# Performance work log

Hardware: AMD Instinct MI355X
Metric: run time of the kernel (lower is better)

Reference implementation:

```python
import jax, jax.numpy as jnp
import numpy as np

ROLLBACK = 1  # rollback_range: warp at 2**rollback finer resolution, then downsample
B, C, H, W = 2, 32, 512, 512
CIN = 3 * (C // 2) + 2  # inner module input channels


def _bilinear_warp(img, res):
    """Bilinear gather. img: [B,Cc,Hh,Ww]; res: [B,Hh,Ww,2] pixel offsets (x,y).
    Samples img at (x+res_x, y+res_y) with zero padding outside."""
    Bb, Cc, Hh, Ww = img.shape
    gy, gx = jnp.meshgrid(jnp.arange(Hh, dtype=img.dtype),
                          jnp.arange(Ww, dtype=img.dtype), indexing='ij')
    sx = gx[None] + res[..., 0]  # [B,Hh,Ww]
    sy = gy[None] + res[..., 1]
    x0 = jnp.floor(sx); y0 = jnp.floor(sy)
    wx = sx - x0; wy = sy - y0

    def gather(yi, xi):
        inb = ((yi >= 0) & (yi < Hh) & (xi >= 0) & (xi < Ww)).astype(img.dtype)
        yc = jnp.clip(yi, 0, Hh - 1).astype(jnp.int32)
        xc = jnp.clip(xi, 0, Ww - 1).astype(jnp.int32)
        v = jax.vmap(lambda im, y, x: im[:, y, x])(img, yc, xc)  # [B,Cc,Hh,Ww]
        return v * inb[:, None]

    v00 = gather(y0, x0);     v01 = gather(y0, x0 + 1)
    v10 = gather(y0 + 1, x0); v11 = gather(y0 + 1, x0 + 1)
    wx = wx[:, None]; wy = wy[:, None]  # broadcast over channels
    return (v00 * (1 - wy) * (1 - wx) + v01 * (1 - wy) * wx
            + v10 * wy * (1 - wx) + v11 * wy * wx)


def _resize_img(img, f):  # [B,Cc,Hh,Ww] bilinear spatial resize
    Bb, Cc, Hh, Ww = img.shape
    return jax.image.resize(img, (Bb, Cc, int(Hh * f), int(Ww * f)), 'bilinear')


def _resize_res(res, f):  # [B,Hh,Ww,2]; pixel-unit values scale with resolution
    Bb, Hh, Ww, _ = res.shape
    return jax.image.resize(res, (Bb, int(Hh * f), int(Ww * f), 2), 'bilinear') * f


def res_warp_img(img, res, rollback):
    if rollback > 0:
        f = 2 ** rollback
        out = _bilinear_warp(_resize_img(img, f), _resize_res(res, f))
        return _resize_img(out, 1.0 / f)
    return _bilinear_warp(img, res)


def res_warp_res(res_a, res_b, rollback):
    # warp residual field a (treated as a 2-channel image, values in pixel units) by b
    if rollback > 0:
        f = 2 ** rollback
        a = _resize_res(res_a, f); b = _resize_res(res_b, f)
        out = jnp.transpose(_bilinear_warp(jnp.transpose(a, (0, 3, 1, 2)), b), (0, 2, 3, 1))
        return _resize_res(out, 1.0 / f)
    out = _bilinear_warp(jnp.transpose(res_a, (0, 3, 1, 2)), res_b)
    return jnp.transpose(out, (0, 2, 3, 1))


def combine_residuals(res_a, res_b, rollback):
    # flow composition: apply a then b
    return res_b + res_warp_res(res_a, res_b, rollback)


def _conv3x3(x, w, b):
    y = jax.lax.conv_general_dilated(x, w, (1, 1), 'SAME',
                                     dimension_numbers=('NCHW', 'OIHW', 'NCHW'))
    return y + b[None, :, None, None]


def setup_inputs() -> dict:
    key = jax.random.key(0)
    k1, k2, k3 = jax.random.split(key, 3)
    x = jax.random.normal(k1, (B, C, H, W), dtype=jnp.float32)
    res = jax.random.normal(k2, (B, 2, H, W), dtype=jnp.float32)  # ~1px flow
    W_inner = jax.random.normal(k3, (2, CIN, 3, 3), dtype=jnp.float32) * 0.02
    b_inner = jnp.zeros((2,), dtype=jnp.float32)
    return {"x": x, "res": res, "W_inner": W_inner, "b_inner": b_inner, "level": 0}


def reference(x, res, W_inner, b_inner, level):
    res_hw = jnp.transpose(res, (0, 2, 3, 1))  # [B,H,W,2]
    nf = x.shape[1]
    src, tgt = x[:, :nf // 2], x[:, nf // 2:]
    warped_tgt = res_warp_img(tgt, res_hw, ROLLBACK)
    bundle = jnp.concatenate([src, tgt, warped_tgt, res], axis=1)  # [B,3C/2+2,H,W]
    adj = _conv3x3(bundle, W_inner, b_inner)  # hindsight_adjustment [B,2,H,W]
    # mode == 'combine_res': state['down'][level]['input'] = combined residual
    new_res = combine_residuals(res_hw, jnp.transpose(adj, (0, 2, 3, 1)), ROLLBACK)
    hindsight_warped_tgt = res_warp_img(tgt, new_res, ROLLBACK)
    return jnp.concatenate([src, hindsight_warped_tgt], axis=1)  # [B,C,H,W]
```

## Files before the change

### kernel.cpp

```cpp
#include <hip/hip_runtime.h>
#include <hip/hip_bf16.h>
#include <cstdint>
#include <cstddef>

#define HW   512
#define HW2  1024
#define SZ   (512 * 512)
#define NPT  (34 * 34)
#define K_PTS 5
#define SRCW 36
#define SRCP 37
#define NSRC (SRCW * SRCW)
#define MARG 9

struct UpTap { int i0, i1; float w0, w1; };

__device__ __forceinline__ UpTap up_tap(int i) {
  UpTap t;
  int k = i >> 1;
  if ((i & 1) == 0) {
    t.i0 = k - 1; t.i1 = k; t.w0 = 0.25f; t.w1 = 0.75f;
    if (k == 0) { t.i0 = 0; t.w0 = 0.0f; t.w1 = 1.0f; }
  } else {
    t.i0 = k; t.i1 = k + 1; t.w0 = 0.75f; t.w1 = 0.25f;
    if (k == HW - 1) { t.i1 = HW - 1; t.w0 = 1.0f; t.w1 = 0.0f; }
  }
  return t;
}

__device__ __forceinline__ float up_at(const float* __restrict__ plane, int yi, int xi) {
  UpTap ty = up_tap(yi), tx = up_tap(xi);
  const float* r0 = plane + (size_t)ty.i0 * HW;
  const float* r1 = plane + (size_t)ty.i1 * HW;
  float v00 = r0[tx.i0], v01 = r0[tx.i1];
  float v10 = r1[tx.i0], v11 = r1[tx.i1];
  return ty.w0 * (tx.w0 * v00 + tx.w1 * v01) + ty.w1 * (tx.w0 * v10 + tx.w1 * v11);
}

__device__ __forceinline__ void axis_taps(float s, int& base, float& w0, float& w1, float& w2) {
  float f0 = floorf(s);
  int i0 = (int)f0;
  float fr = s - f0;
  int b = (i0 & 1) ? (i0 >> 1) : (i0 >> 1) - 1;
  b = b < 0 ? 0 : (b > (HW - 3) ? (HW - 3) : b);
  float w[3] = {0.0f, 0.0f, 0.0f};
  if ((unsigned)i0 < (unsigned)HW2) {
    UpTap t = up_tap(i0);
    w[t.i0 - b] += (1.0f - fr) * t.w0;
    w[t.i1 - b] += (1.0f - fr) * t.w1;
  }
  if ((unsigned)(i0 + 1) < (unsigned)HW2) {
    UpTap t = up_tap(i0 + 1);
    w[t.i0 - b] += fr * t.w0;
    w[t.i1 - b] += fr * t.w1;
  }
  base = b; w0 = w[0]; w1 = w[1]; w2 = w[2];
}

__global__ void copy_src_kernel(const float* __restrict__ x, float* __restrict__ out) {
  const size_t half = (size_t)16 * SZ;
  const size_t nvec = half / 4;
  size_t i = (size_t)blockIdx.x * blockDim.x + threadIdx.x;
  if (i < 2 * nvec) {
    size_t b = i / nvec, j = i % nvec;
    const float4* s = (const float4*)(x + b * 2 * half);
    float4* d = (float4*)(out + b * 2 * half);
    d[j] = s[j];
  }
}

struct PtTaps {
  int   locoff;
  float wy0, wy1, wy2, wx0, wx1, wx2;
};

__device__ __forceinline__ void compute_taps(const float* __restrict__ fx,
                                             const float* __restrict__ fy,
                                             int gx0, int gy0, int xo, int yo, int tid,
                                             PtTaps (&pt)[K_PTS]) {
  #pragma unroll
  for (int i = 0; i < K_PTS; ++i) {
    int p = tid + i * 256;
    pt[i].locoff = 0;
    pt[i].wy0 = pt[i].wy1 = pt[i].wy2 = 0.0f;
    pt[i].wx0 = pt[i].wx1 = pt[i].wx2 = 0.0f;
    if (p < NPT) {
      int ry = p / 34, rx = p % 34;
      int yy = gy0 + ry, xx = gx0 + rx;
      if ((unsigned)yy < (unsigned)HW2 && (unsigned)xx < (unsigned)HW2) {
        float sx = (float)xx + 2.0f * up_at(fx, yy, xx);
        float sy = (float)yy + 2.0f * up_at(fy, yy, xx);
        int bx, by;
        axis_taps(sx, bx, pt[i].wx0, pt[i].wx1, pt[i].wx2);
        axis_taps(sy, by, pt[i].wy0, pt[i].wy1, pt[i].wy2);
        int rx_ = bx - xo, ry_ = by - yo;
        if ((unsigned)rx_ <= (unsigned)(SRCW - 3) && (unsigned)ry_ <= (unsigned)(SRCW - 3))
          pt[i].locoff = ry_ * SRCP + rx_;
        else
          pt[i].locoff = ~(by * HW + bx);
      }
    }
  }
}

__device__ __forceinline__ void stage_pair(const float* __restrict__ p0,
                                           const float* __restrict__ p1,
                                           float* __restrict__ s0,
                                           float* __restrict__ s1,
                                           int xo, int yo, int tid) {
  #pragma unroll
  for (int i = 0; i < 6; ++i) {
    int p = tid + i * 256;
    if (p < NSRC) {
      int r = p / SRCW, c = p % SRCW;
      int gy = yo + r; gy = gy < 0 ? 0 : (gy > HW - 1 ? HW - 1 : gy);
      int gx = xo + c; gx = gx < 0 ? 0 : (gx > HW - 1 ? HW - 1 : gx);
      size_t o = (size_t)gy * HW + gx;
      int d = r * SRCP + c;
      s0[d] = p0[o];
      s1[d] = p1[o];
    }
  }
}

__device__ __forceinline__ float eval3_global(const float* __restrict__ pl, int off, const PtTaps& t) {
  const float* p0 = pl + off;
  float r0 = t.wx0 * p0[0]        + t.wx1 * p0[1]          + t.wx2 * p0[2];
  float r1 = t.wx0 * p0[HW]       + t.wx1 * p0[HW + 1]     + t.wx2 * p0[HW + 2];
  float r2 = t.wx0 * p0[2 * HW]   + t.wx1 * p0[2 * HW + 1] + t.wx2 * p0[2 * HW + 2];
  return t.wy0 * r0 + t.wy1 * r1 + t.wy2 * r2;
}

__device__ __forceinline__ void eval_round(const float* __restrict__ s0,
                                           const float* __restrict__ s1,
                                           float* __restrict__ t0,
                                           float* __restrict__ t1,
                                           const float* __restrict__ plane0,
                                           const float* __restrict__ plane1,
                                           const PtTaps (&pt)[K_PTS], int tid) {
  #pragma unroll
  for (int i = 0; i < K_PTS; ++i) {
    int p = tid + i * 256;
    if (p < NPT) {
      const PtTaps t = pt[i];
      float a0, a1;
      if (t.locoff >= 0) {
        const float* a = s0 + t.locoff;
        const float* b = s1 + t.locoff;
        float r00 = t.wx0 * a[0]        + t.wx1 * a[1]            + t.wx2 * a[2];
        float r10 = t.wx0 * a[SRCP]     + t.wx1 * a[SRCP + 1]     + t.wx2 * a[SRCP + 2];
        float r20 = t.wx0 * a[2 * SRCP] + t.wx1 * a[2 * SRCP + 1] + t.wx2 * a[2 * SRCP + 2];
        float r01 = t.wx0 * b[0]        + t.wx1 * b[1]            + t.wx2 * b[2];
        float r11 = t.wx0 * b[SRCP]     + t.wx1 * b[SRCP + 1]     + t.wx2 * b[SRCP + 2];
        float r21 = t.wx0 * b[2 * SRCP] + t.wx1 * b[2 * SRCP + 1] + t.wx2 * b[2 * SRCP + 2];
        a0 = t.wy0 * r00 + t.wy1 * r10 + t.wy2 * r20;
        a1 = t.wy0 * r01 + t.wy1 * r11 + t.wy2 * r21;
      } else {
        int off = ~t.locoff;
        a0 = eval3_global(plane0, off, t);
        a1 = eval3_global(plane1, off, t);
      }
      t0[p] = a0;
      t1[p] = a1;
    }
  }
}

__global__ void __launch_bounds__(256)
warp_img_kernel(const float* __restrict__ x,
                const float* __restrict__ res,
                float* __restrict__ out)
{
  __shared__ float s_src0[36 * SRCP];
  __shared__ float s_src1[36 * SRCP];
  __shared__ float s_tile0[NPT];
  __shared__ float s_tile1[NPT];

  const int b = blockIdx.z;
  const int tx0 = blockIdx.x * 16, ty0 = blockIdx.y * 16;
  const int gx0 = tx0 * 2 - 1, gy0 = ty0 * 2 - 1;
  const int xo = tx0 - MARG, yo = ty0 - MARG;
  const int tid = threadIdx.x;

  const float* resx = res + (size_t)b * 2 * SZ;
  const float* resy = resx + SZ;
  const float* tgt  = x + ((size_t)b * 32 + 16) * SZ;

  stage_pair(tgt, tgt + SZ, s_src0, s_src1, xo, yo, tid);

  PtTaps pt[K_PTS];
  compute_taps(resx, resy, gx0, gy0, xo, yo, tid, pt);

  const int ly = tid >> 4, lx = tid & 15;
  const int oy = ty0 + ly, ox = tx0 + lx;
  const float RW[4] = {0.25f, 0.75f, 0.75f, 0.25f};
  float wy[4], wx[4];
  float sumy = 0.f, sumx = 0.f;
  #pragma unroll
  for (int d = 0; d < 4; ++d) {
    int g = 2 * oy - 1 + d;
    wy[d] = ((unsigned)g < (unsigned)HW2) ? RW[d] : 0.0f; sumy += wy[d];
    g = 2 * ox - 1 + d;
    wx[d] = ((unsigned)g < (unsigned)HW2) ? RW[d] : 0.0f; sumx += wx[d];
  }
  const float inv = 1.0f / (sumy * sumx);

  __syncthreads();

  for (int c = 0; c < 16; c += 2) {
    const float* plane0 = tgt + (size_t)c * SZ;
    eval_round(s_src0, s_src1, s_tile0, s_tile1, plane0, plane0 + SZ, pt, tid);
    __syncthreads();

    if (c < 14)
      stage_pair(plane0 + 2 * SZ, plane0 + 3 * SZ, s_src0, s_src1, xo, yo, tid);

    float acc0 = 0.0f, acc1 = 0.0f;
    #pragma unroll
    for (int dy = 0; dy < 4; ++dy) {
      float r0 = 0.0f, r1 = 0.0f;
      const int base = (2 * ly + dy) * 34 + 2 * lx;
      #pragma unroll
      for (int dx = 0; dx < 4; ++dx) {
        r0 += wx[dx] * s_tile0[base + dx];
        r1 += wx[dx] * s_tile1[base + dx];
      }
      acc0 += wy[dy] * r0;
      acc1 += wy[dy] * r1;
    }
    size_t o = (((size_t)b * 32 + 16 + c) * HW + oy) * HW + ox;
    out[o] = acc0 * inv;
    out[o + SZ] = acc1 * inv;
    __syncthreads();
  }
}

#define CHN 18
#define CHE (CHN * CHN)

__global__ void __launch_bounds__(256)
conv_kernel(const float* __restrict__ x,
            const float* __restrict__ warped,
            const float* __restrict__ res,
            const float* __restrict__ Wc,
            const float* __restrict__ bc,
            float* __restrict__ adj)
{
  __shared__ float sw[900];
  __shared__ float sh[2][CHE];

  const int tid = threadIdx.x;
  for (int i = tid; i < 900; i += 256) sw[i] = Wc[i];

  const int b = blockIdx.z;
  const int tx0 = blockIdx.x * 16, ty0 = blockIdx.y * 16;
  const int ty = tid >> 4, tx = tid & 15;

  float acc0 = bc[0];
  float acc1 = bc[1];

  const float* px = x + (size_t)b * 32 * SZ;
  const float* pw = warped + ((size_t)b * 32 + 16) * SZ;
  const float* pr = res + (size_t)b * 2 * SZ;

  #define PLANE(ic) ((ic) < 32 ? px + (size_t)(ic) * SZ \
                   : (ic) < 48 ? pw + (size_t)((ic) - 32) * SZ \
                   : pr + (size_t)((ic) - 48) * SZ)

  float rb0, rb1;
  {
    const float* pl = PLANE(0);
    rb0 = 0.f; rb1 = 0.f;
    int p = tid;
    { int ry = p / CHN, rx = p % CHN;
      int gy = ty0 - 1 + ry, gx = tx0 - 1 + rx;
      if ((unsigned)gy < (unsigned)HW && (unsigned)gx < (unsigned)HW) rb0 = pl[(size_t)gy * HW + gx]; }
    p = tid + 256;
    if (p < CHE) {
      int ry = p / CHN, rx = p % CHN;
      int gy = ty0 - 1 + ry, gx = tx0 - 1 + rx;
      if ((unsigned)gy < (unsigned)HW && (unsigned)gx < (unsigned)HW) rb1 = pl[(size_t)gy * HW + gx];
    }
    sh[0][tid] = rb0;
    if (tid + 256 < CHE) sh[0][tid + 256] = rb1;
  }

  for (int ic = 0; ic < 50; ++ic) {
    __syncthreads();
    if (ic < 49) {
      const float* pl = PLANE(ic + 1);
      rb0 = 0.f; rb1 = 0.f;
      int p = tid;
      { int ry = p / CHN, rx = p % CHN;
        int gy = ty0 - 1 + ry, gx = tx0 - 1 + rx;
        if ((unsigned)gy < (unsigned)HW && (unsigned)gx < (unsigned)HW) rb0 = pl[(size_t)gy * HW + gx]; }
      p = tid + 256;
      if (p < CHE) {
        int ry = p / CHN, rx = p % CHN;
        int gy = ty0 - 1 + ry, gx = tx0 - 1 + rx;
        if ((unsigned)gy < (unsigned)HW && (unsigned)gx < (unsigned)HW) rb1 = pl[(size_t)gy * HW + gx];
      }
    }

    const float* hp = sh[ic & 1];
    const float* w0 = &sw[ic * 9];
    const float* w1 = &sw[450 + ic * 9];
    #pragma unroll
    for (int ky = 0; ky < 3; ++ky) {
      #pragma unroll
      for (int kx = 0; kx < 3; ++kx) {
        float v = hp[(ty + ky) * CHN + tx + kx];
        acc0 += v * w0[ky * 3 + kx];
        acc1 += v * w1[ky * 3 + kx];
      }
    }

    if (ic < 49) {
      float* sd = sh[(ic + 1) & 1];
      sd[tid] = rb0;
      if (tid + 256 < CHE) sd[tid + 256] = rb1;
    }
  }
  #undef PLANE

  const int oy = ty0 + ty, ox = tx0 + tx;
  adj[((size_t)b * 2 + 0) * SZ + (size_t)oy * HW + ox] = acc0;
  adj[((size_t)b * 2 + 1) * SZ + (size_t)oy * HW + ox] = acc1;
}

__global__ void __launch_bounds__(256)
new_res_kernel(const float* __restrict__ res,
               const float* __restrict__ adj,
               float* __restrict__ nres)
{
  __shared__ float s_src0[36 * SRCP];
  __shared__ float s_src1[36 * SRCP];
  __shared__ float s_tile0[NPT];
  __shared__ float s_tile1[NPT];

  const int b = blockIdx.z;
  const int tx0 = blockIdx.x * 16, ty0 = blockIdx.y * 16;
  const int gx0 = tx0 * 2 - 1, gy0 = ty0 * 2 - 1;
  const int xo = tx0 - MARG, yo = ty0 - MARG;
  const int tid = threadIdx.x;

  const float* adjx = adj + (size_t)b * 2 * SZ;
  const float* adjy = adjx + SZ;
  const float* res0 = res + (size_t)b * 2 * SZ;
  const float* res1 = res0 + SZ;

  stage_pair(res0, res1, s_src0, s_src1, xo, yo, tid);

  PtTaps pt[K_PTS];
  compute_taps(adjx, adjy, gx0, gy0, xo, yo, tid, pt);

  const int ly = tid >> 4, lx = tid & 15;
  const int oy = ty0 + ly, ox = tx0 + lx;
  const float RW[4] = {0.25f, 0.75f, 0.75f, 0.25f};
  float wy[4], wx[4];
  float sumy = 0.f, sumx = 0.f;
  #pragma unroll
  for (int d = 0; d < 4; ++d) {
    int g = 2 * oy - 1 + d;
    wy[d] = ((unsigned)g < (unsigned)HW2) ? RW[d] : 0.0f; sumy += wy[d];
    g = 2 * ox - 1 + d;
    wx[d] = ((unsigned)g < (unsigned)HW2) ? RW[d] : 0.0f; sumx += wx[d];
  }
  const float inv = 1.0f / (sumy * sumx);

  __syncthreads();
  eval_round(s_src0, s_src1, s_tile0, s_tile1, res0, res1, pt, tid);
  __syncthreads();

  float acc0 = 0.0f, acc1 = 0.0f;
  #pragma unroll
  for (int dy = 0; dy < 4; ++dy) {
    float r0 = 0.0f, r1 = 0.0f;
    const int base = (2 * ly + dy) * 34 + 2 * lx;
    #pragma unroll
    for (int dx = 0; dx < 4; ++dx) {
      r0 += wx[dx] * s_tile0[base + dx];
      r1 += wx[dx] * s_tile1[base + dx];
    }
    acc0 += wy[dy] * r0;
    acc1 += wy[dy] * r1;
  }
  size_t o = ((size_t)b * 2) * SZ + (size_t)oy * HW + ox;
  nres[o]      = acc0 * inv + adjx[(size_t)oy * HW + ox];
  nres[o + SZ] = acc1 * inv + adjy[(size_t)oy * HW + ox];
}

extern "C" void kernel_launch(void* const* d_in, const int* in_sizes, int n_in,
                              void* d_out, int out_size, void* d_ws, size_t ws_size,
                              hipStream_t stream) {
  const float* x   = (const float*)d_in[0];
  const float* res = (const float*)d_in[1];
  const float* Wc  = (const float*)d_in[2];
  const float* bc  = (const float*)d_in[3];
  float* out = (float*)d_out;

  float* adj  = (float*)d_ws;
  float* nres = adj + (size_t)2 * 2 * SZ;

  {
    const size_t nvec = 2 * ((size_t)16 * SZ / 4);
    copy_src_kernel<<<dim3((unsigned)((nvec + 255) / 256)), dim3(256), 0, stream>>>(x, out);
  }

  dim3 tile_grid(32, 32, 2);

  warp_img_kernel<<<tile_grid, dim3(256), 0, stream>>>(x, res, out);

  conv_kernel<<<tile_grid, dim3(256), 0, stream>>>(x, out, res, Wc, bc, adj);

  new_res_kernel<<<tile_grid, dim3(256), 0, stream>>>(res, adj, nres);

  warp_img_kernel<<<tile_grid, dim3(256), 0, stream>>>(x, nres, out);
}
```

Baseline: 408.7 us.

## Fuse src copy into warp kernel, interleave source LDS, deinterleave tile, remap blocks

Removes the separate copy_src kernel by having the first warp_img launch also copy the src channels per pixel as it writes the warped channels. The two staged source planes are interleaved as float2 in shared memory, so each tap fetches both channels in one load. The upsampled tile is stored with even and odd columns split into two halves so the downsampling reads are contiguous and avoid bank conflicts. Blocks use a 1D grid with a swizzle (lin&7)*256+(lin>>3), likely meant to spread neighbouring tiles across XCDs or caches. The cost is extra global traffic inside the warp kernel and a changed block order that may affect cache locality.

```diff
diff --git a/kernel.cpp b/kernel.cpp
--- a/kernel.cpp
+++ b/kernel.cpp
@@ -9,9 +9,11 @@
 #define NPT  (34 * 34)
 #define K_PTS 5
 #define SRCW 36
-#define SRCP 37
+#define SRCP2 37
 #define NSRC (SRCW * SRCW)
 #define MARG 9
+#define TILW 35
+#define NTIL (34 * TILW)
 
 struct UpTap { int i0, i1; float w0, w1; };
 
@@ -55,18 +57,6 @@
     w[t.i1 - b] += fr * t.w1;
   }
   base = b; w0 = w[0]; w1 = w[1]; w2 = w[2];
-}
-
-__global__ void copy_src_kernel(const float* __restrict__ x, float* __restrict__ out) {
-  const size_t half = (size_t)16 * SZ;
-  const size_t nvec = half / 4;
-  size_t i = (size_t)blockIdx.x * blockDim.x + threadIdx.x;
-  if (i < 2 * nvec) {
-    size_t b = i / nvec, j = i % nvec;
-    const float4* s = (const float4*)(x + b * 2 * half);
-    float4* d = (float4*)(out + b * 2 * half);
-    d[j] = s[j];
-  }
 }
 
 struct PtTaps {
@@ -95,7 +85,7 @@
         axis_taps(sy, by, pt[i].wy0, pt[i].wy1, pt[i].wy2);
         int rx_ = bx - xo, ry_ = by - yo;
         if ((unsigned)rx_ <= (unsigned)(SRCW - 3) && (unsigned)ry_ <= (unsigned)(SRCW - 3))
-          pt[i].locoff = ry_ * SRCP + rx_;
+          pt[i].locoff = ry_ * SRCP2 + rx_;
         else
           pt[i].locoff = ~(by * HW + bx);
       }
@@ -105,8 +95,7 @@
 
 __device__ __forceinline__ void stage_pair(const float* __restrict__ p0,
                                            const float* __restrict__ p1,
-                                           float* __restrict__ s0,
-                                           float* __restrict__ s1,
+                                           float2* __restrict__ s,
                                            int xo, int yo, int tid) {
   #pragma unroll
   for (int i = 0; i < 6; ++i) {
@@ -116,9 +105,7 @@
       int gy = yo + r; gy = gy < 0 ? 0 : (gy > HW - 1 ? HW - 1 : gy);
       int gx = xo + c; gx = gx < 0 ? 0 : (gx > HW - 1 ? HW - 1 : gx);
       size_t o = (size_t)gy * HW + gx;
-      int d = r * SRCP + c;
-      s0[d] = p0[o];
-      s1[d] = p1[o];
+      s[r * SRCP2 + c] = make_float2(p0[o], p1[o]);
     }
   }
 }
@@ -131,8 +118,7 @@
   return t.wy0 * r0 + t.wy1 * r1 + t.wy2 * r2;
 }
 
-__device__ __forceinline__ void eval_round(const float* __restrict__ s0,
-                                           const float* __restrict__ s1,
+__device__ __forceinline__ void eval_round(const float2* __restrict__ s_src,
                                            float* __restrict__ t0,
                                            float* __restrict__ t1,
                                            const float* __restrict__ plane0,
@@ -145,14 +131,16 @@
       const PtTaps t = pt[i];
       float a0, a1;
       if (t.locoff >= 0) {
-        const float* a = s0 + t.locoff;
-        const float* b = s1 + t.locoff;
-        float r00 = t.wx0 * a[0]        + t.wx1 * a[1]            + t.wx2 * a[2];
-        float r10 = t.wx0 * a[SRCP]     + t.wx1 * a[SRCP + 1]     + t.wx2 * a[SRCP + 2];
-        float r20 = t.wx0 * a[2 * SRCP] + t.wx1 * a[2 * SRCP + 1] + t.wx2 * a[2 * SRCP + 2];
-        float r01 = t.wx0 * b[0]        + t.wx1 * b[1]            + t.wx2 * b[2];
-        float r11 = t.wx0 * b[SRCP]     + t.wx1 * b[SRCP + 1]     + t.wx2 * b[SRCP + 2];
-        float r21 = t.wx0 * b[2 * SRCP] + t.wx1 * b[2 * SRCP + 1] + t.wx2 * b[2 * SRCP + 2];
+        const float2* s = s_src + t.locoff;
+        float2 v00 = s[0],         v01 = s[1],             v02 = s[2];
+        float2 v10 = s[SRCP2],     v11 = s[SRCP2 + 1],     v12 = s[SRCP2 + 2];
+        float2 v20 = s[2 * SRCP2], v21 = s[2 * SRCP2 + 1], v22 = s[2 * SRCP2 + 2];
+        float r00 = t.wx0 * v00.x + t.wx1 * v01.x + t.wx2 * v02.x;
+        float r10 = t.wx0 * v10.x + t.wx1 * v11.x + t.wx2 * v12.x;
+        float r20 = t.wx0 * v20.x + t.wx1 * v21.x + t.wx2 * v22.x;
+        float r01 = t.wx0 * v00.y + t.wx1 * v01.y + t.wx2 * v02.y;
+        float r11 = t.wx0 * v10.y + t.wx1 * v11.y + t.wx2 * v12.y;
+        float r21 = t.wx0 * v20.y + t.wx1 * v21.y + t.wx2 * v22.y;
         a0 = t.wy0 * r00 + t.wy1 * r10 + t.wy2 * r20;
         a1 = t.wy0 * r01 + t.wy1 * r11 + t.wy2 * r21;
       } else {
@@ -160,8 +148,10 @@
         a0 = eval3_global(plane0, off, t);
         a1 = eval3_global(plane1, off, t);
       }
-      t0[p] = a0;
-      t1[p] = a1;
+      int ry = p / 34, rx = p - ry * 34;
+      int ti = ry * TILW + (rx >> 1) + ((rx & 1) ? 17 : 0);
+      t0[ti] = a0;
+      t1[ti] = a1;
     }
   }
 }
@@ -169,15 +159,18 @@
 __global__ void __launch_bounds__(256)
 warp_img_kernel(const float* __restrict__ x,
                 const float* __restrict__ res,
-                float* __restrict__ out)
+                float* __restrict__ out,
+                int docopy)
 {
-  __shared__ float s_src0[36 * SRCP];
-  __shared__ float s_src1[36 * SRCP];
-  __shared__ float s_tile0[NPT];
-  __shared__ float s_tile1[NPT];
-
-  const int b = blockIdx.z;
-  const int tx0 = blockIdx.x * 16, ty0 = blockIdx.y * 16;
+  __shared__ float2 s_src[36 * SRCP2];
+  __shared__ float  s_tile0[NTIL];
+  __shared__ float  s_tile1[NTIL];
+
+  const int lin = blockIdx.x;
+  const int t = (lin & 7) * 256 + (lin >> 3);
+  const int b = t >> 10;
+  const int by = (t >> 5) & 31, bx = t & 31;
+  const int tx0 = bx * 16, ty0 = by * 16;
   const int gx0 = tx0 * 2 - 1, gy0 = ty0 * 2 - 1;
   const int xo = tx0 - MARG, yo = ty0 - MARG;
   const int tid = threadIdx.x;
@@ -186,7 +179,7 @@
   const float* resy = resx + SZ;
   const float* tgt  = x + ((size_t)b * 32 + 16) * SZ;
 
-  stage_pair(tgt, tgt + SZ, s_src0, s_src1, xo, yo, tid);
+  stage_pair(tgt, tgt + SZ, s_src, xo, yo, tid);
 
   PtTaps pt[K_PTS];
   compute_taps(resx, resy, gx0, gy0, xo, yo, tid, pt);
@@ -204,33 +197,46 @@
     wx[d] = ((unsigned)g < (unsigned)HW2) ? RW[d] : 0.0f; sumx += wx[d];
   }
   const float inv = 1.0f / (sumy * sumx);
+  const size_t pixoff = (size_t)oy * HW + ox;
 
   __syncthreads();
 
   for (int c = 0; c < 16; c += 2) {
     const float* plane0 = tgt + (size_t)c * SZ;
-    eval_round(s_src0, s_src1, s_tile0, s_tile1, plane0, plane0 + SZ, pt, tid);
+    eval_round(s_src, s_tile0, s_tile1, plane0, plane0 + SZ, pt, tid);
     __syncthreads();
 
     if (c < 14)
-      stage_pair(plane0 + 2 * SZ, plane0 + 3 * SZ, s_src0, s_src1, xo, yo, tid);
+      stage_pair(plane0 + 2 * SZ, plane0 + 3 * SZ, s_src, xo, yo, tid);
+
+    float cp0 = 0.f, cp1 = 0.f;
+    if (docopy) {
+      const float* sp = x + ((size_t)b * 32 + c) * SZ + pixoff;
+      cp0 = sp[0];
+      cp1 = sp[SZ];
+    }
 
     float acc0 = 0.0f, acc1 = 0.0f;
     #pragma unroll
     for (int dy = 0; dy < 4; ++dy) {
-      float r0 = 0.0f, r1 = 0.0f;
-      const int base = (2 * ly + dy) * 34 + 2 * lx;
-      #pragma unroll
-      for (int dx = 0; dx < 4; ++dx) {
-        r0 += wx[dx] * s_tile0[base + dx];
-        r1 += wx[dx] * s_tile1[base + dx];
-      }
+      const int rbase = (2 * ly + dy) * TILW;
+      float a0 = s_tile0[rbase + lx],     b0 = s_tile0[rbase + 17 + lx];
+      float c0 = s_tile0[rbase + lx + 1], d0 = s_tile0[rbase + 18 + lx];
+      float a1 = s_tile1[rbase + lx],     b1 = s_tile1[rbase + 17 + lx];
+      float c1 = s_tile1[rbase + lx + 1], d1 = s_tile1[rbase + 18 + lx];
+      float r0 = wx[0] * a0 + wx[1] * b0 + wx[2] * c0 + wx[3] * d0;
+      float r1 = wx[0] * a1 + wx[1] * b1 + wx[2] * c1 + wx[3] * d1;
       acc0 += wy[dy] * r0;
       acc1 += wy[dy] * r1;
     }
-    size_t o = (((size_t)b * 32 + 16 + c) * HW + oy) * HW + ox;
+    size_t o = ((size_t)b * 32 + 16 + c) * SZ + pixoff;
     out[o] = acc0 * inv;
     out[o + SZ] = acc1 * inv;
+    if (docopy) {
+      size_t oc = ((size_t)b * 32 + c) * SZ + pixoff;
+      out[oc] = cp0;
+      out[oc + SZ] = cp1;
+    }
     __syncthreads();
   }
 }
@@ -333,13 +339,15 @@
                const float* __restrict__ adj,
                float* __restrict__ nres)
 {
-  __shared__ float s_src0[36 * SRCP];
-  __shared__ float s_src1[36 * SRCP];
-  __shared__ float s_tile0[NPT];
-  __shared__ float s_tile1[NPT];
-
-  const int b = blockIdx.z;
-  const int tx0 = blockIdx.x * 16, ty0 = blockIdx.y * 16;
+  __shared__ float2 s_src[36 * SRCP2];
+  __shared__ float  s_tile0[NTIL];
+  __shared__ float  s_tile1[NTIL];
+
+  const int lin = blockIdx.x;
+  const int t = (lin & 7) * 256 + (lin >> 3);
+  const int b = t >> 10;
+  const int by = (t >> 5) & 31, bx = t & 31;
+  const int tx0 = bx * 16, ty0 = by * 16;
   const int gx0 = tx0 * 2 - 1, gy0 = ty0 * 2 - 1;
   const int xo = tx0 - MARG, yo = ty0 - MARG;
   const int tid = threadIdx.x;
@@ -349,7 +357,7 @@
   const float* res0 = res + (size_t)b * 2 * SZ;
   const float* res1 = res0 + SZ;
 
-  stage_pair(res0, res1, s_src0, s_src1, xo, yo, tid);
+  stage_pair(res0, res1, s_src, xo, yo, tid);
 
   PtTaps pt[K_PTS];
   compute_taps(adjx, adjy, gx0, gy0, xo, yo, tid, pt);
@@ -369,19 +377,19 @@
   const float inv = 1.0f / (sumy * sumx);
 
   __syncthreads();
-  eval_round(s_src0, s_src1, s_tile0, s_tile1, res0, res1, pt, tid);
+  eval_round(s_src, s_tile0, s_tile1, res0, res1, pt, tid);
   __syncthreads();
 
   float acc0 = 0.0f, acc1 = 0.0f;
   #pragma unroll
   for (int dy = 0; dy < 4; ++dy) {
-    float r0 = 0.0f, r1 = 0.0f;
-    const int base = (2 * ly + dy) * 34 + 2 * lx;
-    #pragma unroll
-    for (int dx = 0; dx < 4; ++dx) {
-      r0 += wx[dx] * s_tile0[base + dx];
-      r1 += wx[dx] * s_tile1[base + dx];
-    }
+    const int rbase = (2 * ly + dy) * TILW;
+    float a0 = s_tile0[rbase + lx],     b0 = s_tile0[rbase + 17 + lx];
+    float c0 = s_tile0[rbase + lx + 1], d0 = s_tile0[rbase + 18 + lx];
+    float a1 = s_tile1[rbase + lx],     b1 = s_tile1[rbase + 17 + lx];
+    float c1 = s_tile1[rbase + lx + 1], d1 = s_tile1[rbase + 18 + lx];
+    float r0 = wx[0] * a0 + wx[1] * b0 + wx[2] * c0 + wx[3] * d0;
+    float r1 = wx[0] * a1 + wx[1] * b1 + wx[2] * c1 + wx[3] * d1;
     acc0 += wy[dy] * r0;
     acc1 += wy[dy] * r1;
   }
@@ -402,18 +410,11 @@
   float* adj  = (float*)d_ws;
   float* nres = adj + (size_t)2 * 2 * SZ;
 
-  {
-    const size_t nvec = 2 * ((size_t)16 * SZ / 4);
-    copy_src_kernel<<<dim3((unsigned)((nvec + 255) / 256)), dim3(256), 0, stream>>>(x, out);
-  }
-
-  dim3 tile_grid(32, 32, 2);
-
-  warp_img_kernel<<<tile_grid, dim3(256), 0, stream>>>(x, res, out);
-
-  conv_kernel<<<tile_grid, dim3(256), 0, stream>>>(x, out, res, Wc, bc, adj);
-
-  new_res_kernel<<<tile_grid, dim3(256), 0, stream>>>(res, adj, nres);
-
-  warp_img_kernel<<<tile_grid, dim3(256), 0, stream>>>(x, nres, out);
-}
+  warp_img_kernel<<<dim3(2048), dim3(256), 0, stream>>>(x, res, out, 1);
+
+  conv_kernel<<<dim3(32, 32, 2), dim3(256), 0, stream>>>(x, out, res, Wc, bc, adj);
+
+  new_res_kernel<<<dim3(2048), dim3(256), 0, stream>>>(res, adj, nres);
+
+  warp_img_kernel<<<dim3(2048), dim3(256), 0, stream>>>(x, nres, out, 0);
+}
```

Result: slower. 440.7 us (+7.8%).
